# Kernel tuning notes

Measured on AMD Instinct MI355X. Metric: run time of the kernel, lower is better.

The kernel has to match this reference:

```python
import jax, jax.numpy as jnp
import numpy as np

N_NODE = 100000
N_EDGE = 1600000
D_FEAT = 32
DEPTH = 10
BASE_ALPHA = 1.0


def setup_inputs() -> dict:
    key = jax.random.key(0)
    k1, k2, k3, k4 = jax.random.split(key, 4)
    x = jax.random.normal(k1, (N_NODE, D_FEAT), dtype=jnp.float32)
    edge_index = jax.random.randint(k2, (2, N_EDGE), 0, N_NODE, dtype=jnp.int64)
    edge_attr = jax.random.uniform(k3, (N_EDGE,), dtype=jnp.float32)
    pe_alphas = jax.random.normal(k4, (DEPTH,), dtype=jnp.float32)
    return {"x": x, "edge_index": edge_index, "edge_attr": edge_attr, "pe_alphas": pe_alphas}


def reference(x, edge_index, edge_attr, pe_alphas):
    n = x.shape[0]
    row, col = edge_index[0], edge_index[1]
    # GCN normalization: deg from row (source of each edge), clamp isolated nodes
    deg = jax.ops.segment_sum(jnp.ones_like(edge_attr), row, num_segments=n)
    deg = jnp.where(deg < 0.5, deg + 1.0, deg)
    dinv = deg ** -0.5
    val = dinv[row] * edge_attr * dinv[col]  # [E]

    alphas = BASE_ALPHA * jnp.tanh(pe_alphas)  # [DEPTH]

    def spmm(h):  # adj @ h via gather + segment-sum scatter
        return jax.ops.segment_sum(val[:, None] * h[col], row, num_segments=n)

    # PowerConv (monomial basis): x_L = alpha_{L-1} * (adj @ x_{L-1}), x_0 = x
    def step(h, a):
        nh = a * spmm(h)
        return nh, nh

    _, ys = jax.lax.scan(step, x, alphas)  # ys: [DEPTH, n, d]
    out = jnp.concatenate([x[None], ys], axis=0)  # [DEPTH+1, n, d]
    return jnp.moveaxis(out, 0, 1)  # [n, DEPTH+1, d]
```

## Files before the change

kernel.cpp:

```cpp
#include <hip/hip_runtime.h>

#define NN 100000
#define NE 1600000
#define DF 32
#define DEPTH 10
#define LSTRIDE ((DEPTH + 1) * DF)
#define SCAN_BLOCKS 256
#define SCAN_T 256

__global__ void fill_k(int* __restrict__ cnt, int4* __restrict__ cpack4,
                       int n4_cnt, long long cp4) {
    long long i = (long long)blockIdx.x * blockDim.x + threadIdx.x;
    long long stride = (long long)gridDim.x * blockDim.x;
    const int4 z = make_int4(0, 0, 0, 0);
    for (long long j = i; j < cp4; j += stride) cpack4[j] = z;
    int4* c4 = (int4*)cnt;
    for (long long j = i; j < n4_cnt; j += stride) c4[j] = z;
}

__global__ void hist_k(const int* __restrict__ row, int* __restrict__ cnt,
                       int* __restrict__ prank, int e) {
    int i = blockIdx.x * blockDim.x + threadIdx.x;
    int stride = gridDim.x * blockDim.x;
    for (; i < e; i += stride) {
        int r = __builtin_nontemporal_load(&row[i]);
        prank[i] = atomicAdd(&cnt[r], 1);
    }
}

__global__ void scan_partial_k(const int* __restrict__ cnt, int* __restrict__ bsum,
                               int n, int chunk) {
    __shared__ int red[SCAN_T];
    int b = blockIdx.x, t = threadIdx.x;
    int beg = b * chunk, end = min(n, beg + chunk);
    int s = 0;
    for (int i = beg + t; i < end; i += SCAN_T) s += (cnt[i] + 7) & ~7;
    red[t] = s;
    __syncthreads();
    for (int off = SCAN_T / 2; off; off >>= 1) {
        if (t < off) red[t] += red[t + off];
        __syncthreads();
    }
    if (t == 0) bsum[b] = red[0];
}

__global__ void scan_bsum_k(const int* __restrict__ bsum, int* __restrict__ boff) {
    __shared__ int s[SCAN_BLOCKS];
    int t = threadIdx.x;
    s[t] = bsum[t];
    __syncthreads();
    for (int off = 1; off < SCAN_BLOCKS; off <<= 1) {
        int v = (t >= off) ? s[t - off] : 0;
        __syncthreads();
        s[t] += v;
        __syncthreads();
    }
    boff[t] = (t == 0) ? 0 : s[t - 1];
}

__global__ void scan_emit_k(const int* __restrict__ cnt, const int* __restrict__ boff,
                            int* __restrict__ rowptr, float* __restrict__ dinv,
                            int n, int chunk) {
    __shared__ int tile[SCAN_T];
    int b = blockIdx.x, t = threadIdx.x;
    int beg = b * chunk, end = min(n, beg + chunk);
    int run = boff[b];
    for (int base = beg; base < end; base += SCAN_T) {
        int i = base + t;
        int creal = (i < end) ? cnt[i] : 0;
        int c = (creal + 7) & ~7;
        tile[t] = c;
        __syncthreads();
        for (int off = 1; off < SCAN_T; off <<= 1) {
            int v = (t >= off) ? tile[t - off] : 0;
            __syncthreads();
            tile[t] += v;
            __syncthreads();
        }
        if (i < end) {
            rowptr[i] = run + tile[t] - c;
            float d = (creal == 0) ? 1.0f : (float)creal;
            dinv[i] = rsqrtf(d);
        }
        run += tile[SCAN_T - 1];
        __syncthreads();
    }
    if (b == gridDim.x - 1 && t == 0) rowptr[n] = run;
}

__global__ void scatter_k(const int* __restrict__ row, const int* __restrict__ col,
                          const float* __restrict__ ea, const float* __restrict__ dinv,
                          const int* __restrict__ rowptr, const int* __restrict__ prank,
                          int2* __restrict__ cpack, int e) {
    int i = blockIdx.x * blockDim.x + threadIdx.x;
    int stride = gridDim.x * blockDim.x;
    for (; i < e; i += stride) {
        int r = __builtin_nontemporal_load(&row[i]);
        int c = __builtin_nontemporal_load(&col[i]);
        float a = __builtin_nontemporal_load(&ea[i]);
        int pr = __builtin_nontemporal_load(&prank[i]);
        float v = dinv[r] * a * dinv[c];
        int pos = rowptr[r] + pr;
        cpack[pos] = make_int2(c, __float_as_int(v));
    }
}

__global__ void copy_k(const float* __restrict__ x, float* __restrict__ out, int n) {
    int t = blockIdx.x * blockDim.x + threadIdx.x;
    if (t < n * 8) {
        int node = t >> 3, q = t & 7;
        ((float4*)out)[(size_t)node * (LSTRIDE / 4) + q] = ((const float4*)x)[t];
    }
}

__global__ __launch_bounds__(256) void spmm_k(const int* __restrict__ rowptr,
                                              const unsigned long long* __restrict__ cpack,
                                              const float* __restrict__ pe,
                                              float* __restrict__ out, int n, int layer) {
    int lane = threadIdx.x & 31;
    int g0 = blockIdx.x * 8 + (threadIdx.x >> 5);
    int gstride = gridDim.x * 8;
    float alpha = tanhf(pe[layer]);
    const float* __restrict__ hsrc = out + (size_t)layer * DF + lane;
    for (int gid = g0; gid < n; gid += gstride) {
        int beg = rowptr[gid], end = rowptr[gid + 1];
        float acc = 0.f;
        for (int base = beg; base < end; base += 8) {
            unsigned long long p[8];
#pragma unroll
            for (int u = 0; u < 8; ++u) p[u] = __builtin_nontemporal_load(&cpack[base + u]);
            float h[8];
#pragma unroll
            for (int u = 0; u < 8; ++u)
                h[u] = hsrc[(unsigned)(p[u] & 0xFFFFFFFFu) * (unsigned)LSTRIDE];
#pragma unroll
            for (int u = 0; u < 8; ++u)
                acc = fmaf(__uint_as_float((unsigned)(p[u] >> 32)), h[u], acc);
        }
        out[(size_t)gid * LSTRIDE + (layer + 1) * DF + lane] = alpha * acc;
    }
}

extern "C" void kernel_launch(void* const* d_in, const int* in_sizes, int n_in,
                              void* d_out, int out_size, void* d_ws, size_t ws_size,
                              hipStream_t stream) {
    const float* x  = (const float*)d_in[0];
    const int*   ei = (const int*)d_in[1];
    const float* ea = (const float*)d_in[2];
    const float* pe = (const float*)d_in[3];
    float* out = (float*)d_out;

    const int n = in_sizes[0] / DF;
    const int e = in_sizes[2];
    const int* row = ei;
    const int* col = ei + e;

    int*   cnt    = (int*)d_ws;
    int*   rowptr = cnt + n;
    float* dinv   = (float*)(rowptr + n + 1);
    int*   bsum   = (int*)(dinv + n);
    int*   boff   = bsum + SCAN_BLOCKS;
    int*   prank  = boff + SCAN_BLOCKS;
    size_t off = ((size_t)(prank + e) - (size_t)d_ws + 15) & ~(size_t)15;
    int2*  cpack = (int2*)((char*)d_ws + off);

    const long long cpack_entries = (long long)e + 7ll * n;
    const long long cp4 = (cpack_entries * 2 + 3) / 4;
    const int n4_cnt = (n + 3) / 4;

    const int chunk = (n + SCAN_BLOCKS - 1) / SCAN_BLOCKS;

    fill_k<<<2048, 256, 0, stream>>>(cnt, (int4*)cpack, n4_cnt, cp4);
    hist_k<<<2048, 256, 0, stream>>>(row, cnt, prank, e);
    scan_partial_k<<<SCAN_BLOCKS, SCAN_T, 0, stream>>>(cnt, bsum, n, chunk);
    scan_bsum_k<<<1, SCAN_BLOCKS, 0, stream>>>(bsum, boff);
    scan_emit_k<<<SCAN_BLOCKS, SCAN_T, 0, stream>>>(cnt, boff, rowptr, dinv, n, chunk);
    scatter_k<<<2048, 256, 0, stream>>>(row, col, ea, dinv, rowptr, prank, cpack, e);
    copy_k<<<(n * 8 + 255) / 256, 256, 0, stream>>>(x, out, n);

    for (int L = 0; L < DEPTH; ++L) {
        spmm_k<<<2048, 256, 0, stream>>>(rowptr, (const unsigned long long*)cpack,
                                         pe, out, n, L);
    }
}
```

Measured before the change: 576.2 us.

## Gather bf16 copies of layer features from compact ping-pong buffers in SpMM

Each layer now writes a bf16 copy of its output into a dense n×32 ping-pong buffer, and the next layer gathers neighbor features from that compact bf16 array instead of from the strided fp32 output tensor. This halves the bytes per random gather and packs the working set densely so it fits in cache better. The grid also changes to one warp-group per node with no grid-stride loop. Because every propagated value is rounded to bf16, error compounds over ten layers and may break the accuracy tolerance.

```diff
diff --git a/kernel.cpp b/kernel.cpp
--- a/kernel.cpp
+++ b/kernel.cpp
@@ -105,40 +105,55 @@
     }
 }
 
-__global__ void copy_k(const float* __restrict__ x, float* __restrict__ out, int n) {
+__device__ __forceinline__ unsigned short f32_to_bf16(float f) {
+    unsigned b = __float_as_uint(f);
+    b += 0x7FFFu + ((b >> 16) & 1u);
+    return (unsigned short)(b >> 16);
+}
+
+__global__ void copy_k(const float* __restrict__ x, float* __restrict__ out,
+                       unsigned short* __restrict__ hb0, int n) {
     int t = blockIdx.x * blockDim.x + threadIdx.x;
     if (t < n * 8) {
         int node = t >> 3, q = t & 7;
-        ((float4*)out)[(size_t)node * (LSTRIDE / 4) + q] = ((const float4*)x)[t];
+        float4 v = ((const float4*)x)[t];
+        ((float4*)out)[(size_t)node * (LSTRIDE / 4) + q] = v;
+        ushort4 h;
+        h.x = f32_to_bf16(v.x); h.y = f32_to_bf16(v.y);
+        h.z = f32_to_bf16(v.z); h.w = f32_to_bf16(v.w);
+        ((ushort4*)hb0)[t] = h;
     }
 }
 
 __global__ __launch_bounds__(256) void spmm_k(const int* __restrict__ rowptr,
                                               const unsigned long long* __restrict__ cpack,
                                               const float* __restrict__ pe,
+                                              const unsigned short* __restrict__ hin,
+                                              unsigned short* __restrict__ hout,
                                               float* __restrict__ out, int n, int layer) {
+    int gid = blockIdx.x * 8 + (threadIdx.x >> 5);
     int lane = threadIdx.x & 31;
-    int g0 = blockIdx.x * 8 + (threadIdx.x >> 5);
-    int gstride = gridDim.x * 8;
+    if (gid >= n) return;
     float alpha = tanhf(pe[layer]);
-    const float* __restrict__ hsrc = out + (size_t)layer * DF + lane;
-    for (int gid = g0; gid < n; gid += gstride) {
-        int beg = rowptr[gid], end = rowptr[gid + 1];
-        float acc = 0.f;
-        for (int base = beg; base < end; base += 8) {
-            unsigned long long p[8];
+    const unsigned short* __restrict__ hsrc = hin + lane;
+    int beg = rowptr[gid], end = rowptr[gid + 1];
+    float acc = 0.f;
+    for (int base = beg; base < end; base += 8) {
+        unsigned long long p[8];
 #pragma unroll
-            for (int u = 0; u < 8; ++u) p[u] = __builtin_nontemporal_load(&cpack[base + u]);
-            float h[8];
+        for (int u = 0; u < 8; ++u) p[u] = __builtin_nontemporal_load(&cpack[base + u]);
+        unsigned short h[8];
 #pragma unroll
-            for (int u = 0; u < 8; ++u)
-                h[u] = hsrc[(unsigned)(p[u] & 0xFFFFFFFFu) * (unsigned)LSTRIDE];
+        for (int u = 0; u < 8; ++u)
+            h[u] = hsrc[(unsigned)(p[u] & 0xFFFFFFFFu) * (unsigned)DF];
 #pragma unroll
-            for (int u = 0; u < 8; ++u)
-                acc = fmaf(__uint_as_float((unsigned)(p[u] >> 32)), h[u], acc);
-        }
-        out[(size_t)gid * LSTRIDE + (layer + 1) * DF + lane] = alpha * acc;
-    }
+        for (int u = 0; u < 8; ++u)
+            acc = fmaf(__uint_as_float((unsigned)(p[u] >> 32)),
+                       __uint_as_float((unsigned)h[u] << 16), acc);
+    }
+    float r = alpha * acc;
+    out[(size_t)gid * LSTRIDE + (layer + 1) * DF + lane] = r;
+    hout[(unsigned)gid * DF + lane] = f32_to_bf16(r);
 }
 
 extern "C" void kernel_launch(void* const* d_in, const int* in_sizes, int n_in,
@@ -163,8 +178,10 @@
     int*   prank  = boff + SCAN_BLOCKS;
     size_t off = ((size_t)(prank + e) - (size_t)d_ws + 15) & ~(size_t)15;
     int2*  cpack = (int2*)((char*)d_ws + off);
-
     const long long cpack_entries = (long long)e + 7ll * n;
+    unsigned short* hb0 = (unsigned short*)(cpack + cpack_entries);
+    unsigned short* hb1 = hb0 + (size_t)n * DF;
+
     const long long cp4 = (cpack_entries * 2 + 3) / 4;
     const int n4_cnt = (n + 3) / 4;
 
@@ -176,10 +193,12 @@
     scan_bsum_k<<<1, SCAN_BLOCKS, 0, stream>>>(bsum, boff);
     scan_emit_k<<<SCAN_BLOCKS, SCAN_T, 0, stream>>>(cnt, boff, rowptr, dinv, n, chunk);
     scatter_k<<<2048, 256, 0, stream>>>(row, col, ea, dinv, rowptr, prank, cpack, e);
-    copy_k<<<(n * 8 + 255) / 256, 256, 0, stream>>>(x, out, n);
+    copy_k<<<(n * 8 + 255) / 256, 256, 0, stream>>>(x, out, hb0, n);
 
     for (int L = 0; L < DEPTH; ++L) {
-        spmm_k<<<2048, 256, 0, stream>>>(rowptr, (const unsigned long long*)cpack,
-                                         pe, out, n, L);
-    }
-}
+        unsigned short* hin  = (L & 1) ? hb1 : hb0;
+        unsigned short* hout = (L & 1) ? hb0 : hb1;
+        spmm_k<<<(n + 7) / 8, 256, 0, stream>>>(rowptr, (const unsigned long long*)cpack,
+                                                pe, hin, hout, out, n, L);
+    }
+}
```

After: 567.1 us. About the same (-1.6%).
